# Optimization experiments

Hardware: AMD Instinct MI355X
Metric: run time of the kernel (lower is better)

The kernel has to match this reference:

```python
import jax, jax.numpy as jnp
import numpy as np

NUM_F = 8
IN_DIM = 768
OUT_DIM = 768
B = 64
N = 196


def setup_inputs() -> dict:
    key = jax.random.key(0)
    ks = jax.random.split(key, 6)
    x = jax.random.normal(ks[0], (B, N, IN_DIM), dtype=jnp.float32)
    base_weight = jax.random.normal(ks[1], (OUT_DIM, IN_DIM), dtype=jnp.float32) * (IN_DIM ** -0.5)
    grid = jnp.arange(NUM_F, dtype=jnp.float32) + 1.0  # torch.arange(num_f)+1
    scale_sp = jnp.ones((OUT_DIM,), dtype=jnp.float32)
    coef = jax.random.uniform(ks[2], (IN_DIM, NUM_F), dtype=jnp.float32)
    conv_w = jax.random.normal(ks[3], (NUM_F, OUT_DIM, IN_DIM), dtype=jnp.float32) * (IN_DIM ** -0.5)
    conv_b = jax.random.normal(ks[4], (NUM_F, OUT_DIM), dtype=jnp.float32) * 0.01
    return {"x": x, "base_weight": base_weight, "grid": grid, "scale_sp": scale_sp,
            "coef": coef, "conv_w": conv_w, "conv_b": conv_b}


def reference(x, base_weight, grid, scale_sp, coef, conv_w, conv_b):
    b, n, d = x.shape
    xf = x.reshape(b * n, d)  # [batch, in_dim]
    # base path: SiLU then linear
    base_out = jax.nn.silu(xf) @ base_weight.T  # [batch, out_dim]
    # spline path: sin(grid_f * x) weighted by per-(feature,freq) coef
    # s: [batch, num_f, in_dim]
    s = jnp.sin(xf[:, None, :] * grid[None, :, None]) * coef.T[None, :, :]
    # grouped 1x1 conv == per-frequency block matmul: [batch, num_f, out_dim]
    spline = jnp.einsum('bfi,foi->bfo', s, conv_w) + conv_b[None, :, :]
    out = base_out + spline.sum(axis=1) * scale_sp
    return out.reshape(b, n, OUT_DIM)
```

## Files before the change

### kernel.cpp

```cpp
#include <hip/hip_runtime.h>

#define M_TOTAL 12544
#define IN_D 768
#define OUT_D 768
#define NUM_F 8
#define NP 9
#define KTOT (IN_D * NP)

#define BM 128
#define BN 128
#define BK 32
#define MT_TILES (M_TOTAL / BM)
#define NT_TILES (OUT_D / BN)
#define PJ (IN_D / BK)
#define KT_TILES (KTOT / BK)
#define GRANA 512

typedef __attribute__((ext_vector_type(8))) short short8;
typedef __attribute__((ext_vector_type(4))) float f32x4;

__device__ __forceinline__ unsigned short f2bf(float f) {
  unsigned u = __float_as_uint(f);
  u += 0x7fff + ((u >> 16) & 1);
  return (unsigned short)(u >> 16);
}

__global__ __launch_bounds__(256) void pack_a_t(
    const float* __restrict__ x, const float* __restrict__ grid,
    const float* __restrict__ coef, short8* __restrict__ At)
{
  __shared__ float xs[32][129];
  __shared__ float cs[32][8];

  const int bid = blockIdx.x;
  const int mt = bid / PJ, jj = bid % PJ;
  const int tid = threadIdx.x;

  {
    const int c = tid & 7;
    const int r0 = tid >> 3;
    #pragma unroll
    for (int q = 0; q < 4; ++q) {
      int r = q * 32 + r0;
      f32x4 v = *(const f32x4*)(x + (size_t)(mt * 128 + r) * IN_D + jj * 32 + c * 4);
      #pragma unroll
      for (int e = 0; e < 4; ++e) xs[c * 4 + e][r] = v[e];
    }
  }
  cs[tid >> 3][tid & 7] = coef[(size_t)(jj * 32 + (tid >> 3)) * NUM_F + (tid & 7)];
  __syncthreads();

  for (int p = 0; p < NP; ++p) {
    short8* dst = At + ((size_t)mt * KT_TILES + p * PJ + jj) * GRANA;
    float gf = (p > 0) ? grid[p - 1] : 0.f;
    #pragma unroll
    for (int c2 = 0; c2 < 2; ++c2) {
      int g = c2 * 256 + tid;
      int row = g & 127, kc = g >> 7;
      short8 s;
      if (p == 0) {
        #pragma unroll
        for (int e = 0; e < 8; ++e) {
          float t = xs[kc * 8 + e][row];
          s[e] = (short)f2bf(t / (1.f + __expf(-t)));
        }
      } else {
        #pragma unroll
        for (int e = 0; e < 8; ++e) {
          float t = xs[kc * 8 + e][row];
          s[e] = (short)f2bf(__sinf(t * gf) * cs[kc * 8 + e][p - 1]);
        }
      }
      dst[g] = s;
    }
  }
}

__global__ __launch_bounds__(256) void pack_b_t(
    const float* __restrict__ bw, const float* __restrict__ ssp,
    const float* __restrict__ cw, short8* __restrict__ Bt)
{
  int gg = blockIdx.x * 256 + threadIdx.x;
  int nt = gg / (KT_TILES * GRANA);
  int rem = gg % (KT_TILES * GRANA);
  int kt = rem >> 9;
  int g = rem & 511;
  int row = g & 127, kc = g >> 7;
  int o = nt * 128 + row;
  int p = kt / PJ, jj = kt % PJ;
  int i0 = jj * 32 + kc * 8;
  const float* src = (p == 0) ? bw + (size_t)o * IN_D + i0
                              : cw + ((size_t)(p - 1) * OUT_D + o) * IN_D + i0;
  float fac = (p == 0) ? 1.f : ssp[o];
  f32x4 v0 = ((const f32x4*)src)[0], v1 = ((const f32x4*)src)[1];
  short8 s;
  #pragma unroll
  for (int e = 0; e < 4; ++e) {
    s[e]     = (short)f2bf(v0[e] * fac);
    s[e + 4] = (short)f2bf(v1[e] * fac);
  }
  Bt[gg] = s;
}

__global__ __launch_bounds__(256, 4) void skan_gemm(
    const short8* __restrict__ At, const short8* __restrict__ Bt,
    const float* __restrict__ ssp, const float* __restrict__ cb,
    float* __restrict__ out)
{
  __shared__ short8 Asm[2][GRANA];
  __shared__ short8 Bsm[2][GRANA];
  __shared__ float bias_sm[BN];

  const int bid0 = blockIdx.x;
  const int xcd = bid0 & 7;
  const int idx = bid0 >> 3;
  const int wgid = (xcd < 4 ? xcd * 74 : 4 * 74 + (xcd - 4) * 73) + idx;
  const int tm = wgid / NT_TILES, tn = wgid % NT_TILES;
  const int m0 = tm * BM, n0 = tn * BN;

  const int tid = threadIdx.x;
  const int lane = tid & 63, wid = tid >> 6;
  const int wm = wid >> 1, wn = wid & 1;
  const int lrow = lane & 15, lkb = lane >> 4;

  if (tid < BN) {
    int o = n0 + tid;
    float s = 0.f;
    #pragma unroll
    for (int f = 0; f < NUM_F; ++f) s += cb[f * OUT_D + o];
    bias_sm[tid] = s * ssp[o];
  }

  const short8* Abase = At + (size_t)tm * KT_TILES * GRANA;
  const short8* Bbase = Bt + (size_t)tn * KT_TILES * GRANA;

  auto STAGE = [&](int buf, int t) {
    const short8* as = Abase + (size_t)t * GRANA;
    const short8* bs = Bbase + (size_t)t * GRANA;
    #pragma unroll
    for (int c = 0; c < 2; ++c) {
      __builtin_amdgcn_global_load_lds(
          (const __attribute__((address_space(1))) void*)(as + c * 256 + tid),
          (__attribute__((address_space(3))) void*)&Asm[buf][c * 256 + tid],
          16, 0, 0);
      __builtin_amdgcn_global_load_lds(
          (const __attribute__((address_space(1))) void*)(bs + c * 256 + tid),
          (__attribute__((address_space(3))) void*)&Bsm[buf][c * 256 + tid],
          16, 0, 0);
    }
  };

  f32x4 acc[4][4];
  #pragma unroll
  for (int i = 0; i < 4; ++i)
    #pragma unroll
    for (int j = 0; j < 4; ++j)
      acc[i][j] = (f32x4){0.f, 0.f, 0.f, 0.f};

  STAGE(0, 0);
  for (int t = 0; t < KT_TILES; ++t) {
    const int cur = t & 1;
    __syncthreads();
    if (t + 1 < KT_TILES) STAGE(cur ^ 1, t + 1);
    short8 af[4], bfr[4];
    #pragma unroll
    for (int q = 0; q < 4; ++q) {
      int base = lkb * 128 + q * 16 + lrow;
      af[q]  = Asm[cur][base + wm * 64];
      bfr[q] = Bsm[cur][base + wn * 64];
    }
    #pragma unroll
    for (int i = 0; i < 4; ++i)
      #pragma unroll
      for (int j = 0; j < 4; ++j)
        acc[i][j] = __builtin_amdgcn_mfma_f32_16x16x32_bf16(af[i], bfr[j], acc[i][j], 0, 0, 0);
  }

  #pragma unroll
  for (int i = 0; i < 4; ++i) {
    int row = m0 + wm * 64 + i * 16 + lkb * 4;
    #pragma unroll
    for (int j = 0; j < 4; ++j) {
      int col = n0 + wn * 64 + j * 16 + lrow;
      float bia = bias_sm[wn * 64 + j * 16 + lrow];
      float* op = out + (size_t)row * OUT_D + col;
      op[0 * OUT_D] = acc[i][j][0] + bia;
      op[1 * OUT_D] = acc[i][j][1] + bia;
      op[2 * OUT_D] = acc[i][j][2] + bia;
      op[3 * OUT_D] = acc[i][j][3] + bia;
    }
  }
}

extern "C" void kernel_launch(void* const* d_in, const int* in_sizes, int n_in,
                              void* d_out, int out_size, void* d_ws, size_t ws_size,
                              hipStream_t stream) {
  (void)in_sizes; (void)n_in; (void)out_size; (void)ws_size;
  const float* x    = (const float*)d_in[0];
  const float* bw   = (const float*)d_in[1];
  const float* grid = (const float*)d_in[2];
  const float* ssp  = (const float*)d_in[3];
  const float* coef = (const float*)d_in[4];
  const float* cw   = (const float*)d_in[5];
  const float* cb   = (const float*)d_in[6];
  float* out = (float*)d_out;

  const size_t A_bytes = (size_t)MT_TILES * KT_TILES * GRANA * 16;
  short8* Aw = (short8*)d_ws;
  short8* Bw = (short8*)((char*)d_ws + A_bytes);

  pack_a_t<<<MT_TILES * PJ, 256, 0, stream>>>(x, grid, coef, Aw);
  pack_b_t<<<(NT_TILES * KT_TILES * GRANA) / 256, 256, 0, stream>>>(bw, ssp, cw, Bw);
  skan_gemm<<<MT_TILES * NT_TILES, 256, 0, stream>>>(Aw, Bw, ssp, cb, out);
}
```

Before: 297.0 us.

## Fuse activation packing into GEMM and fold coef into packed weights

Removes the separate A-packing kernel and its large bf16 workspace. The GEMM now streams raw x tiles into LDS, computes SiLU and sin(grid*x) on the fly, and writes bf16 A fragments to LDS. The K order is interleaved per 32-column chunk over the nine paths so each x tile is reused across all paths. The per-(feature,freq) coef is folded into the packed B weights. This cuts global A traffic, but adds transcendental math inside the GEMM loop and lowers the occupancy hint to 2 blocks per CU. Each x tile is recomputed once for every N tile.

Measured after the change: 408.1 us. 37.4% more time.

```diff
diff --git a/kernel.cpp b/kernel.cpp
--- a/kernel.cpp
+++ b/kernel.cpp
@@ -25,60 +25,10 @@
   return (unsigned short)(u >> 16);
 }
 
-__global__ __launch_bounds__(256) void pack_a_t(
-    const float* __restrict__ x, const float* __restrict__ grid,
-    const float* __restrict__ coef, short8* __restrict__ At)
-{
-  __shared__ float xs[32][129];
-  __shared__ float cs[32][8];
-
-  const int bid = blockIdx.x;
-  const int mt = bid / PJ, jj = bid % PJ;
-  const int tid = threadIdx.x;
-
-  {
-    const int c = tid & 7;
-    const int r0 = tid >> 3;
-    #pragma unroll
-    for (int q = 0; q < 4; ++q) {
-      int r = q * 32 + r0;
-      f32x4 v = *(const f32x4*)(x + (size_t)(mt * 128 + r) * IN_D + jj * 32 + c * 4);
-      #pragma unroll
-      for (int e = 0; e < 4; ++e) xs[c * 4 + e][r] = v[e];
-    }
-  }
-  cs[tid >> 3][tid & 7] = coef[(size_t)(jj * 32 + (tid >> 3)) * NUM_F + (tid & 7)];
-  __syncthreads();
-
-  for (int p = 0; p < NP; ++p) {
-    short8* dst = At + ((size_t)mt * KT_TILES + p * PJ + jj) * GRANA;
-    float gf = (p > 0) ? grid[p - 1] : 0.f;
-    #pragma unroll
-    for (int c2 = 0; c2 < 2; ++c2) {
-      int g = c2 * 256 + tid;
-      int row = g & 127, kc = g >> 7;
-      short8 s;
-      if (p == 0) {
-        #pragma unroll
-        for (int e = 0; e < 8; ++e) {
-          float t = xs[kc * 8 + e][row];
-          s[e] = (short)f2bf(t / (1.f + __expf(-t)));
-        }
-      } else {
-        #pragma unroll
-        for (int e = 0; e < 8; ++e) {
-          float t = xs[kc * 8 + e][row];
-          s[e] = (short)f2bf(__sinf(t * gf) * cs[kc * 8 + e][p - 1]);
-        }
-      }
-      dst[g] = s;
-    }
-  }
-}
-
 __global__ __launch_bounds__(256) void pack_b_t(
     const float* __restrict__ bw, const float* __restrict__ ssp,
-    const float* __restrict__ cw, short8* __restrict__ Bt)
+    const float* __restrict__ cw, const float* __restrict__ coef,
+    short8* __restrict__ Bt)
 {
   int gg = blockIdx.x * 256 + threadIdx.x;
   int nt = gg / (KT_TILES * GRANA);
@@ -87,26 +37,36 @@
   int g = rem & 511;
   int row = g & 127, kc = g >> 7;
   int o = nt * 128 + row;
-  int p = kt / PJ, jj = kt % PJ;
+  int jj = kt / NP, p = kt % NP;
   int i0 = jj * 32 + kc * 8;
-  const float* src = (p == 0) ? bw + (size_t)o * IN_D + i0
-                              : cw + ((size_t)(p - 1) * OUT_D + o) * IN_D + i0;
-  float fac = (p == 0) ? 1.f : ssp[o];
-  f32x4 v0 = ((const f32x4*)src)[0], v1 = ((const f32x4*)src)[1];
   short8 s;
-  #pragma unroll
-  for (int e = 0; e < 4; ++e) {
-    s[e]     = (short)f2bf(v0[e] * fac);
-    s[e + 4] = (short)f2bf(v1[e] * fac);
+  if (p == 0) {
+    const float* src = bw + (size_t)o * IN_D + i0;
+    f32x4 v0 = ((const f32x4*)src)[0], v1 = ((const f32x4*)src)[1];
+    #pragma unroll
+    for (int e = 0; e < 4; ++e) {
+      s[e]     = (short)f2bf(v0[e]);
+      s[e + 4] = (short)f2bf(v1[e]);
+    }
+  } else {
+    const float* src = cw + ((size_t)(p - 1) * OUT_D + o) * IN_D + i0;
+    float fac = ssp[o];
+    f32x4 v0 = ((const f32x4*)src)[0], v1 = ((const f32x4*)src)[1];
+    #pragma unroll
+    for (int e = 0; e < 4; ++e) {
+      s[e]     = (short)f2bf(v0[e] * fac * coef[(size_t)(i0 + e) * NUM_F + (p - 1)]);
+      s[e + 4] = (short)f2bf(v1[e] * fac * coef[(size_t)(i0 + 4 + e) * NUM_F + (p - 1)]);
+    }
   }
   Bt[gg] = s;
 }
 
-__global__ __launch_bounds__(256, 4) void skan_gemm(
-    const short8* __restrict__ At, const short8* __restrict__ Bt,
-    const float* __restrict__ ssp, const float* __restrict__ cb,
-    float* __restrict__ out)
+__global__ __launch_bounds__(256, 2) void skan_fused_gemm(
+    const float* __restrict__ x, const float* __restrict__ grid,
+    const short8* __restrict__ Bt, const float* __restrict__ ssp,
+    const float* __restrict__ cb, float* __restrict__ out)
 {
+  __shared__ __align__(16) float xs[128 * 32];
   __shared__ short8 Asm[2][GRANA];
   __shared__ short8 Bsm[2][GRANA];
   __shared__ float bias_sm[BN];
@@ -122,6 +82,8 @@
   const int lane = tid & 63, wid = tid >> 6;
   const int wm = wid >> 1, wn = wid & 1;
   const int lrow = lane & 15, lkb = lane >> 4;
+  const int row_t = tid & 127;
+  const int kc0 = (tid >> 7) * 2;
 
   if (tid < BN) {
     int o = n0 + tid;
@@ -131,25 +93,60 @@
     bias_sm[tid] = s * ssp[o];
   }
 
-  const short8* Abase = At + (size_t)tm * KT_TILES * GRANA;
-  const short8* Bbase = Bt + (size_t)tn * KT_TILES * GRANA;
-
-  auto STAGE = [&](int buf, int t) {
-    const short8* as = Abase + (size_t)t * GRANA;
-    const short8* bs = Bbase + (size_t)t * GRANA;
-    #pragma unroll
-    for (int c = 0; c < 2; ++c) {
-      __builtin_amdgcn_global_load_lds(
-          (const __attribute__((address_space(1))) void*)(as + c * 256 + tid),
-          (__attribute__((address_space(3))) void*)&Asm[buf][c * 256 + tid],
-          16, 0, 0);
-      __builtin_amdgcn_global_load_lds(
-          (const __attribute__((address_space(1))) void*)(bs + c * 256 + tid),
-          (__attribute__((address_space(3))) void*)&Bsm[buf][c * 256 + tid],
-          16, 0, 0);
-    }
-  };
-
+  float gv[8];
+  #pragma unroll
+  for (int p = 0; p < 8; ++p) gv[p] = grid[p];
+
+#define STAGE_X(jjn)                                                          \
+  { _Pragma("unroll") for (int k = 0; k < 4; ++k) {                           \
+      int rrow = k * 32 + (tid >> 3);                                         \
+      int cphys = tid & 7;                                                    \
+      int clog = (cphys - rrow) & 7;                                          \
+      const float* sxp = x + (size_t)(m0 + rrow) * IN_D + (jjn) * 32 + clog * 4; \
+      __builtin_amdgcn_global_load_lds(                                       \
+          (const __attribute__((address_space(1))) void*)sxp,                 \
+          (__attribute__((address_space(3))) void*)&xs[k * 1024 + tid * 4],   \
+          16, 0, 0);                                                          \
+    } }
+
+#define READ_XR(arr)                                                          \
+  { _Pragma("unroll") for (int q = 0; q < 4; ++q) {                           \
+      int cphys = ((kc0 * 2 + q) + row_t) & 7;                                \
+      arr[q] = *(const f32x4*)&xs[row_t * 32 + cphys * 4];                    \
+    } }
+
+#define ACT(pn, arr, d0, d1)                                                  \
+  {                                                                           \
+    if ((pn) == 0) {                                                          \
+      _Pragma("unroll") for (int e = 0; e < 4; ++e) {                         \
+        float t0 = arr[0][e], t1 = arr[1][e], t2 = arr[2][e], t3 = arr[3][e]; \
+        d0[e]     = (short)f2bf(t0 / (1.f + __expf(-t0)));                    \
+        d0[e + 4] = (short)f2bf(t1 / (1.f + __expf(-t1)));                    \
+        d1[e]     = (short)f2bf(t2 / (1.f + __expf(-t2)));                    \
+        d1[e + 4] = (short)f2bf(t3 / (1.f + __expf(-t3)));                    \
+      }                                                                       \
+    } else {                                                                  \
+      float gg = gv[(pn) - 1];                                                \
+      _Pragma("unroll") for (int e = 0; e < 4; ++e) {                         \
+        d0[e]     = (short)f2bf(__sinf(arr[0][e] * gg));                      \
+        d0[e + 4] = (short)f2bf(__sinf(arr[1][e] * gg));                      \
+        d1[e]     = (short)f2bf(__sinf(arr[2][e] * gg));                      \
+        d1[e + 4] = (short)f2bf(__sinf(arr[3][e] * gg));                      \
+      }                                                                       \
+    }                                                                         \
+  }
+
+#define STAGE_B(buf, bsrc)                                                    \
+  { _Pragma("unroll") for (int c = 0; c < 2; ++c) {                           \
+      __builtin_amdgcn_global_load_lds(                                       \
+          (const __attribute__((address_space(1))) void*)((bsrc) + c * 256 + tid), \
+          (__attribute__((address_space(3))) void*)&Bsm[buf][c * 256 + tid],  \
+          16, 0, 0);                                                          \
+    } }
+
+  const short8* bptr = Bt + (size_t)tn * KT_TILES * GRANA;
+
+  f32x4 xr[4], yr[4];
   f32x4 acc[4][4];
   #pragma unroll
   for (int i = 0; i < 4; ++i)
@@ -157,23 +154,51 @@
     for (int j = 0; j < 4; ++j)
       acc[i][j] = (f32x4){0.f, 0.f, 0.f, 0.f};
 
-  STAGE(0, 0);
-  for (int t = 0; t < KT_TILES; ++t) {
-    const int cur = t & 1;
-    __syncthreads();
-    if (t + 1 < KT_TILES) STAGE(cur ^ 1, t + 1);
-    short8 af[4], bfr[4];
-    #pragma unroll
-    for (int q = 0; q < 4; ++q) {
-      int base = lkb * 128 + q * 16 + lrow;
-      af[q]  = Asm[cur][base + wm * 64];
-      bfr[q] = Bsm[cur][base + wn * 64];
-    }
-    #pragma unroll
-    for (int i = 0; i < 4; ++i)
+  STAGE_X(0);
+  STAGE_B(0, bptr);
+  __syncthreads();
+  READ_XR(xr);
+  {
+    short8 a0, a1;
+    ACT(0, xr, a0, a1);
+    Asm[0][kc0 * 128 + row_t] = a0;
+    Asm[0][(kc0 + 1) * 128 + row_t] = a1;
+  }
+
+  int t = 0;
+  for (int jj = 0; jj < PJ; ++jj) {
+    #pragma unroll
+    for (int p = 0; p < 9; ++p, ++t) {
+      const int cur = t & 1;
+      const int nxt = cur ^ 1;
+      __syncthreads();
+      if (t + 1 < KT_TILES) {
+        if (p == 2 && jj < PJ - 1) STAGE_X(jj + 1);
+        STAGE_B(nxt, bptr + (size_t)(t + 1) * GRANA);
+        if (p == 7 && jj < PJ - 1) READ_XR(yr);
+        short8 a0, a1;
+        if (p < 8) { ACT(p + 1, xr, a0, a1); }
+        else       { ACT(0, yr, a0, a1); }
+        Asm[nxt][kc0 * 128 + row_t] = a0;
+        Asm[nxt][(kc0 + 1) * 128 + row_t] = a1;
+      }
+      short8 af[4], bfr[4];
       #pragma unroll
-      for (int j = 0; j < 4; ++j)
-        acc[i][j] = __builtin_amdgcn_mfma_f32_16x16x32_bf16(af[i], bfr[j], acc[i][j], 0, 0, 0);
+      for (int q = 0; q < 4; ++q) {
+        int base = lkb * 128 + q * 16 + lrow;
+        af[q]  = Asm[cur][base + wm * 64];
+        bfr[q] = Bsm[cur][base + wn * 64];
+      }
+      #pragma unroll
+      for (int i = 0; i < 4; ++i)
+        #pragma unroll
+        for (int j = 0; j < 4; ++j)
+          acc[i][j] = __builtin_amdgcn_mfma_f32_16x16x32_bf16(af[i], bfr[j], acc[i][j], 0, 0, 0);
+    }
+    if (jj < PJ - 1) {
+      #pragma unroll
+      for (int q = 0; q < 4; ++q) xr[q] = yr[q];
+    }
   }
 
   #pragma unroll
@@ -190,6 +215,10 @@
       op[3 * OUT_D] = acc[i][j][3] + bia;
     }
   }
+#undef STAGE_X
+#undef READ_XR
+#undef ACT
+#undef STAGE_B
 }
 
 extern "C" void kernel_launch(void* const* d_in, const int* in_sizes, int n_in,
@@ -205,11 +234,10 @@
   const float* cb   = (const float*)d_in[6];
   float* out = (float*)d_out;
 
-  const size_t A_bytes = (size_t)MT_TILES * KT_TILES * GRANA * 16;
-  short8* Aw = (short8*)d_ws;
-  short8* Bw = (short8*)((char*)d_ws + A_bytes);
-
-  pack_a_t<<<MT_TILES * PJ, 256, 0, stream>>>(x, grid, coef, Aw);
-  pack_b_t<<<(NT_TILES * KT_TILES * GRANA) / 256, 256, 0, stream>>>(bw, ssp, cw, Bw);
-  skan_gemm<<<MT_TILES * NT_TILES, 256, 0, stream>>>(Aw, Bw, ssp, cb, out);
-}
+  short8* Bw = (short8*)d_ws;
+
+  pack_b_t<<<(NT_TILES * KT_TILES * GRANA) / 256, 256, 0, stream>>>(
+      bw, ssp, cw, coef, Bw);
+  skan_fused_gemm<<<MT_TILES * NT_TILES, 256, 0, stream>>>(
+      x, grid, Bw, ssp, cb, out);
+}
```
